# Optimization experiments

Hardware: AMD Instinct MI355X
Metric: run time of the kernel (lower is better)

Reference implementation:

```python
import jax, jax.numpy as jnp
import numpy as np

B, S = 2, 1024
IN, OUT = 1024, 1024
N_IN, N_OUT = 32, 32          # isqrt(IN), isqrt(OUT)
CD = 64                       # compressed_feature_dim
K = 2                         # num_monarchs
D1 = N_IN * N_IN * N_OUT      # 32768, flat M1 size per token
D2 = N_OUT * N_IN * N_OUT     # 32768, flat M2 size per token


def setup_inputs() -> dict:
    key = jax.random.key(0)
    ks = jax.random.split(key, 13)
    g = lambda k, shape, s=0.02: jax.random.normal(k, shape, dtype=jnp.float32) * s
    return {
        "x":  jax.random.normal(ks[0], (B, S, IN), dtype=jnp.float32),
        "Wc": g(ks[1], (IN, CD)),  "bc": g(ks[2], (CD,)),
        "W1": g(ks[3], (K, CD, D1)), "b1": g(ks[4], (K, D1)),
        "W2": g(ks[5], (K, CD, D2)), "b2": g(ks[6], (K, D2)),
        "Wm": g(ks[7], (CD, K)),   "bm": g(ks[8], (K,)),
        "Wb": g(ks[9], (CD, OUT)), "bb": g(ks[10], (OUT,)),
        "Wr": g(ks[11], (CD, 1)),  "br": g(ks[12], (1,)),
    }


def reference(x, Wc, bc, W1, b1, W2, b2, Wm, bm, Wb, bb, Wr, br):
    b, s, _ = x.shape
    # compressor: Linear + Tanh -> [B,S,CD]
    cf = jnp.tanh(x @ Wc + bc)
    # per-expert generated flat weights: [B,S,K,D]
    gen1 = jnp.einsum('bsc,kcd->bskd', cf, W1) + b1
    gen2 = jnp.einsum('bsc,kcd->bskd', cf, W2) + b2
    # expert mixing coefficients -> softmax over K
    coeffs = jax.nn.softmax(cf @ Wm + bm, axis=-1)  # [B,S,K]
    M1f = jnp.einsum('bskd,bsk->bsd', gen1, coeffs)
    M2f = jnp.einsum('bskd,bsk->bsd', gen2, coeffs)
    # Monarch block matmul with per-token weights
    M1 = M1f.reshape(b, s, N_IN, N_IN, N_OUT)   # g=N_IN blocks of [N_IN,N_OUT]
    M2 = M2f.reshape(b, s, N_OUT, N_IN, N_OUT)  # g=N_OUT blocks of [N_IN,N_OUT]
    x1 = x.reshape(b, s, N_IN, N_IN)
    h1 = jnp.einsum('bsgi,bsgio->bsgo', x1, M1)      # [B,S,N_IN,N_OUT]
    h1t = jnp.swapaxes(h1, -1, -2)                   # [B,S,N_OUT,N_IN]
    h2 = jnp.einsum('bsgi,bsgio->bsgo', h1t, M2)     # [B,S,N_OUT,N_OUT]
    y = h2.reshape(b, s, OUT)
    # per-token scale and bias
    ratio = cf @ Wr + br                             # [B,S,1]
    bias = cf @ Wb + bb                              # [B,S,OUT]
    return y * ratio + bias
```

## Files before the change

### kernel.cpp

```cpp
#include <hip/hip_runtime.h>
#include <cstddef>

typedef unsigned short ushortT;
typedef short s8v __attribute__((ext_vector_type(8)));
typedef float f32x4 __attribute__((ext_vector_type(4)));

constexpr int NTOK = 2048;

__device__ inline ushortT f2bf(float f) {
  unsigned u = __float_as_uint(f);
  u += 0x7fffu + ((u >> 16) & 1u);
  return (ushortT)(u >> 16);
}

__device__ inline void gl_lds16(const s8v* g, s8v* l) {
  __builtin_amdgcn_global_load_lds(
      (const __attribute__((address_space(1))) unsigned int*)g,
      (__attribute__((address_space(3))) unsigned int*)l, 16, 0, 0);
}

__global__ __launch_bounds__(256) void setup_kernel(
    const float* __restrict__ x, const float* __restrict__ Wc, const float* __restrict__ bc,
    const float* __restrict__ Wm, const float* __restrict__ bm,
    const float* __restrict__ Wr, const float* __restrict__ br,
    const float* __restrict__ W1, const float* __restrict__ b1,
    const float* __restrict__ W2, const float* __restrict__ b2,
    const float* __restrict__ Wb, const float* __restrict__ bb,
    ushortT* __restrict__ FP, float* __restrict__ ratio,
    ushortT* __restrict__ P1, ushortT* __restrict__ P2, ushortT* __restrict__ WbP)
{
  __shared__ __align__(16) char smem[16384];
  const int tid = threadIdx.x;
  const int bid = blockIdx.x;

  if (bid < 512) {
    float* part = (float*)smem;
    float* cf_s = part + 1024;
    float* a0s  = cf_s + 256;
    float* a1s  = a0s + 4;
    const int c = tid & 63;
    const int q = tid >> 6;
    const int t0 = bid * 4;

    float acc[4];
#pragma unroll
    for (int p = 0; p < 4; ++p) acc[p] = 0.f;
    const float* xq = x + (size_t)t0 * 1024 + q * 256;
    const float* wq = Wc + (size_t)(q * 256) * 64 + c;
#pragma unroll 4
    for (int jj = 0; jj < 64; ++jj) {
      float w0 = wq[(jj * 4 + 0) * 64];
      float w1 = wq[(jj * 4 + 1) * 64];
      float w2 = wq[(jj * 4 + 2) * 64];
      float w3 = wq[(jj * 4 + 3) * 64];
#pragma unroll
      for (int p = 0; p < 4; ++p) {
        float4 xv = *(const float4*)(xq + (size_t)p * 1024 + jj * 4);
        acc[p] = fmaf(xv.x, w0, acc[p]);
        acc[p] = fmaf(xv.y, w1, acc[p]);
        acc[p] = fmaf(xv.z, w2, acc[p]);
        acc[p] = fmaf(xv.w, w3, acc[p]);
      }
    }
#pragma unroll
    for (int p = 0; p < 4; ++p) part[(q * 4 + p) * 64 + c] = acc[p];
    __syncthreads();

    {
      int p = tid >> 6, cc = tid & 63;
      float s = part[(0 + p) * 64 + cc] + part[(4 + p) * 64 + cc] +
                part[(8 + p) * 64 + cc] + part[(12 + p) * 64 + cc] + bc[cc];
      cf_s[p * 64 + cc] = tanhf(s);
    }
    __syncthreads();

    {
      float cf = cf_s[q * 64 + c];
      float z0 = cf * Wm[2 * c], z1 = cf * Wm[2 * c + 1], rr = cf * Wr[c];
      for (int off = 32; off; off >>= 1) {
        z0 += __shfl_down(z0, off);
        z1 += __shfl_down(z1, off);
        rr += __shfl_down(rr, off);
      }
      if (c == 0) {
        z0 += bm[0]; z1 += bm[1];
        float mx = fmaxf(z0, z1);
        float e0 = expf(z0 - mx), e1 = expf(z1 - mx);
        float a0 = e0 / (e0 + e1);
        a0s[q] = a0;
        a1s[q] = 1.0f - a0;
        ratio[t0 + q] = rr + br[0];
      }
    }
    __syncthreads();

    const int ks0 = c >> 5, kk = c & 31;
    const int slot = (kk >> 3) * 16, e = kk & 7;
    {
      int t = t0 + q, tt = t >> 4, tok = t & 15;
      size_t base = (size_t)tt * 2560;
      float cf = cf_s[q * 64 + c];
      float a0 = a0s[q], a1 = a1s[q];
      FP[base + (size_t)ks0 * 512 + (slot + tok) * 8 + e]       = f2bf(a0 * cf);
      FP[base + (size_t)(2 + ks0) * 512 + (slot + tok) * 8 + e] = f2bf(a1 * cf);
      if (c < 32) {
        float v = (c == 0) ? a0 : (c == 1) ? a1 : 0.0f;
        FP[base + 4 * 512 + ((c >> 3) * 16 + tok) * 8 + (c & 7)] = f2bf(v);
      }
    }
  } else {
    ushortT (*lds)[1024] = (ushortT (*)[1024])smem;
    int pb = bid - 512;
    int fac, g, jc8;
    if (pb < 1280) { fac = pb / 640; int rem = pb % 640; g = rem / 20; jc8 = rem % 20; }
    else           { fac = 2; g = 0; jc8 = pb - 1280; }
    const float* W  = (fac == 0) ? W1 : W2;
    const float* bv = (fac == 0) ? b1 : b2;
    ushortT* P = (fac == 0) ? P1 : (fac == 1) ? P2 : WbP;
    const int c4 = tid;

#pragma unroll
    for (int rl = 0; rl < 8; ++rl) {
      int jj = jc8 * 8 + rl;
      float4 v = make_float4(0.f, 0.f, 0.f, 0.f);
      if (fac < 2) {
        if (jj < 128)       v = *(const float4*)(W  + (size_t)jj * 32768 + g * 1024 + c4 * 4);
        else if (jj < 130)  v = *(const float4*)(bv + (size_t)(jj - 128) * 32768 + g * 1024 + c4 * 4);
      } else {
        if (jj < 128)       v = *(const float4*)(Wb + (size_t)(jj & 63) * 1024 + c4 * 4);
        else if (jj < 130)  v = *(const float4*)(bb + c4 * 4);
      }
      int col0 = c4 * 4;
      int sw = col0 ^ ((col0 >> 4) & 0x1C);
      ushortT* d = &lds[rl][sw];
      d[0] = f2bf(v.x); d[1] = f2bf(v.y); d[2] = f2bf(v.z); d[3] = f2bf(v.w);
    }
    __syncthreads();
    const int ks = jc8 >> 2, kkg = jc8 & 3;
#pragma unroll
    for (int it = 0; it < 4; ++it) {
      int idx = tid + it * 256;
      int ct_l = idx >> 4, cl = idx & 15;
      int scol;
      if (fac < 2) {
        int o = ct_l >> 1, ib = (ct_l & 1) * 16;
        scol = (ib + cl) * 32 + o;
      } else {
        scol = ct_l * 16 + cl;
      }
      scol ^= ((scol >> 4) & 0x1C);
      ushortT v[8];
#pragma unroll
      for (int e = 0; e < 8; ++e) v[e] = lds[e][scol];
      size_t ctile = (fac < 2) ? (size_t)(g * 64 + ct_l) : (size_t)ct_l;
      size_t off = ctile * 2560 + (size_t)ks * 512 + (kkg * 16 + cl) * 8;
      uint4 qv;
      qv.x = v[0] | ((unsigned)v[1] << 16);
      qv.y = v[2] | ((unsigned)v[3] << 16);
      qv.z = v[4] | ((unsigned)v[5] << 16);
      qv.w = v[6] | ((unsigned)v[7] << 16);
      *(uint4*)(P + off) = qv;
    }
  }
}

template <int PASS>
__global__ __launch_bounds__(256, 2) void mm_kernel(
    const s8v* __restrict__ fP, const s8v* __restrict__ wP,
    const s8v* __restrict__ wbP,
    const float* __restrict__ xg,
    const float* __restrict__ rat,
    float* __restrict__ outp)
{
  __shared__ s8v bsh[2][1280];
  __shared__ float xsf[(PASS == 1 ? 2 : 1) * 2112];
  __shared__ float hs[PASS == 2 ? 64 : 1][9];
  __shared__ float bls[PASS == 2 ? 64 : 1][9];
  const int tid = threadIdx.x;
  const int lane = tid & 63;
  const int w = tid >> 6;
  const int bid = blockIdx.x;
  const int cb  = (bid & 7) * 16 + (bid >> 5);
  const int tbgh = (bid >> 3) & 3;
  const int g = cb >> 2;

  const s8v* ap = wP + (size_t)(cb * 16 + w * 4) * 320 + lane;
  s8v a[4][5];
#pragma unroll
  for (int i = 0; i < 4; ++i)
#pragma unroll
    for (int ks = 0; ks < 5; ++ks) a[i][ks] = ap[i * 320 + ks * 64];

  s8v ab[5];
  if constexpr (PASS == 2) {
    const s8v* abp = wbP + (size_t)(cb >> 1) * 320 + lane;
#pragma unroll
    for (int ks = 0; ks < 5; ++ks) ab[ks] = abp[ks * 64];
  }

  const s8v* fbase = fP + (size_t)(tbgh * 8) * 1280;

#pragma unroll
  for (int c2 = 0; c2 < 5; ++c2)
    gl_lds16(fbase + w * 320 + c2 * 64 + lane, &bsh[0][w * 320 + c2 * 64]);
  __syncthreads();

#pragma unroll 1
  for (int tt2 = 0; tt2 < 8; ++tt2) {
    const int buf = tt2 & 1;
    const int t0 = (tbgh * 8 + tt2) * 64;

    float4 xv[2];
#pragma unroll
    for (int it = 0; it < 2; ++it) {
      int idx = tid + it * 256;
      if (PASS == 1) {
        int t = idx >> 3, i4 = idx & 7;
        xv[it] = *(const float4*)(xg + (size_t)(t0 + t) * 1024 + g * 32 + i4 * 4);
      } else {
        int i = idx >> 4, tq = idx & 15;
        xv[it] = *(const float4*)(xg + (size_t)(i * 32 + g) * 2048 + t0 + tq * 4);
      }
    }
    if (tt2 < 7) {
      const s8v* fn = fbase + (size_t)(tt2 + 1) * 1280;
#pragma unroll
      for (int c2 = 0; c2 < 5; ++c2)
        gl_lds16(fn + w * 320 + c2 * 64 + lane, &bsh[buf ^ 1][w * 320 + c2 * 64]);
    }

    f32x4 acc[4][4];
#pragma unroll
    for (int i = 0; i < 4; ++i)
#pragma unroll
      for (int j = 0; j < 4; ++j) acc[i][j] = {0.f, 0.f, 0.f, 0.f};
    f32x4 accb = {0.f, 0.f, 0.f, 0.f};

    __builtin_amdgcn_s_setprio(1);
#pragma unroll
    for (int ks = 0; ks < 5; ++ks) {
      s8v b0 = bsh[buf][0 * 320 + ks * 64 + lane];
      s8v b1 = bsh[buf][1 * 320 + ks * 64 + lane];
      s8v b2 = bsh[buf][2 * 320 + ks * 64 + lane];
      s8v b3 = bsh[buf][3 * 320 + ks * 64 + lane];
      if constexpr (PASS == 2) {
        s8v bw = bsh[buf][w * 320 + ks * 64 + lane];
        accb = __builtin_amdgcn_mfma_f32_16x16x32_bf16(ab[ks], bw, accb, 0, 0, 0);
      }
#pragma unroll
      for (int i = 0; i < 4; ++i) {
        acc[i][0] = __builtin_amdgcn_mfma_f32_16x16x32_bf16(a[i][ks], b0, acc[i][0], 0, 0, 0);
        acc[i][1] = __builtin_amdgcn_mfma_f32_16x16x32_bf16(a[i][ks], b1, acc[i][1], 0, 0, 0);
        acc[i][2] = __builtin_amdgcn_mfma_f32_16x16x32_bf16(a[i][ks], b2, acc[i][2], 0, 0, 0);
        acc[i][3] = __builtin_amdgcn_mfma_f32_16x16x32_bf16(a[i][ks], b3, acc[i][3], 0, 0, 0);
      }
    }
    __builtin_amdgcn_s_setprio(0);

#pragma unroll
    for (int it = 0; it < 2; ++it) {
      int idx = tid + it * 256;
      float* d;
      if (PASS == 1) { int t = idx >> 3, i4 = idx & 7; d = &xsf[buf * 2112 + t * 33 + i4 * 4]; }
      else           { int i = idx >> 4, tq = idx & 15; d = &xsf[i * 66 + tq * 4]; }
      d[0] = xv[it].x; d[1] = xv[it].y; d[2] = xv[it].z; d[3] = xv[it].w;
    }
    __syncthreads();

    const int tau = lane & 15, q = lane >> 4;
#pragma unroll
    for (int tt = 0; tt < 4; ++tt) {
      int tl = tt * 16 + tau;
#pragma unroll
      for (int run = 0; run < 2; ++run) {
        float sacc = 0.f;
#pragma unroll
        for (int ch = 0; ch < 2; ++ch) {
          int ct = run * 2 + ch;
          f32x4 av = acc[ct][tt];
#pragma unroll
          for (int r = 0; r < 4; ++r) {
            int i = ch * 16 + q * 4 + r;
            float xvv = (PASS == 1) ? xsf[buf * 2112 + tl * 33 + i] : xsf[i * 66 + tl];
            sacc = fmaf(av[r], xvv, sacc);
          }
        }
        sacc += __shfl_xor(sacc, 16);
        sacc += __shfl_xor(sacc, 32);
        if constexpr (PASS == 1) {
          if (lane < 16) {
            int colg = g * 32 + (cb & 3) * 8 + w * 2 + run;
            outp[(size_t)colg * 2048 + t0 + tt * 16 + tau] = sacc;
          }
        } else {
          if (lane < 16) hs[tl][w * 2 + run] = sacc;
        }
      }
    }
    if constexpr (PASS == 2) {
      if ((lane >> 5) == (cb & 1)) {
        int ol = ((lane >> 4) & 1) * 4;
#pragma unroll
        for (int r = 0; r < 4; ++r) bls[w * 16 + tau][ol + r] = accb[r];
      }
      __syncthreads();
      if (tid < 128) {
        int row = tid >> 1, half = tid & 1;
        int t = t0 + row;
        int col = g * 32 + (cb & 3) * 8 + half * 4;
        float r = rat[t];
        float4 o;
        o.x = fmaf(hs[row][half * 4 + 0], r, bls[row][half * 4 + 0]);
        o.y = fmaf(hs[row][half * 4 + 1], r, bls[row][half * 4 + 1]);
        o.z = fmaf(hs[row][half * 4 + 2], r, bls[row][half * 4 + 2]);
        o.w = fmaf(hs[row][half * 4 + 3], r, bls[row][half * 4 + 3]);
        *(float4*)(outp + (size_t)t * 1024 + col) = o;
      }
    }
  }
}

extern "C" void kernel_launch(void* const* d_in, const int* in_sizes, int n_in,
                              void* d_out, int out_size, void* d_ws, size_t ws_size,
                              hipStream_t stream) {
  const float* x  = (const float*)d_in[0];
  const float* Wc = (const float*)d_in[1];
  const float* bc = (const float*)d_in[2];
  const float* W1 = (const float*)d_in[3];
  const float* b1 = (const float*)d_in[4];
  const float* W2 = (const float*)d_in[5];
  const float* b2 = (const float*)d_in[6];
  const float* Wm = (const float*)d_in[7];
  const float* bm = (const float*)d_in[8];
  const float* Wb = (const float*)d_in[9];
  const float* bb = (const float*)d_in[10];
  const float* Wr = (const float*)d_in[11];
  const float* br = (const float*)d_in[12];
  float* out = (float*)d_out;

  ushortT* P1  = (ushortT*)d_ws;
  ushortT* P2  = P1 + (size_t)2048 * 2560;
  ushortT* WbP = P2 + (size_t)2048 * 2560;
  ushortT* FP  = WbP + (size_t)64 * 2560;
  float* ratio = (float*)(FP + (size_t)128 * 2560);
  float* h1T   = ratio + NTOK;

  setup_kernel<<<dim3(1812), dim3(256), 0, stream>>>(
      x, Wc, bc, Wm, bm, Wr, br, W1, b1, W2, b2, Wb, bb, FP, ratio, P1, P2, WbP);
  mm_kernel<1><<<dim3(512), dim3(256), 0, stream>>>(
      (const s8v*)FP, (const s8v*)P1, (const s8v*)WbP, x, nullptr, h1T);
  mm_kernel<2><<<dim3(512), dim3(256), 0, stream>>>(
      (const s8v*)FP, (const s8v*)P2, (const s8v*)WbP, h1T, ratio, out);
}
```

Before: 77.13 us.

## Move W2 and Wb packing from setup kernel into pass-1 matmul launch

Packing of the W2/b2 and Wb/bb weights into bf16 MFMA tile layout moves out of the setup kernel and into extra blocks appended to the pass-1 matmul grid. The setup grid shrinks, and the W2/Wb packing can run alongside the pass-1 MFMA work, shortening the serial critical path. The pack blocks reuse the matmul's LDS buffer and return early. They compete with matmul blocks for CUs and bandwidth, and the pass-1 grid now contains two kinds of block with very different costs.

```diff
diff --git a/kernel.cpp b/kernel.cpp
--- a/kernel.cpp
+++ b/kernel.cpp
@@ -17,6 +17,57 @@
   __builtin_amdgcn_global_load_lds(
       (const __attribute__((address_space(1))) unsigned int*)g,
       (__attribute__((address_space(3))) unsigned int*)l, 16, 0, 0);
+}
+
+__device__ inline void pack_slab(
+    ushortT (*lds)[1024], int tid, int fac, int g, int jc8,
+    const float* __restrict__ W, const float* __restrict__ bv,
+    const float* __restrict__ Wb, const float* __restrict__ bb,
+    ushortT* __restrict__ P)
+{
+  const int c4 = tid;
+#pragma unroll
+  for (int rl = 0; rl < 8; ++rl) {
+    int jj = jc8 * 8 + rl;
+    float4 v = make_float4(0.f, 0.f, 0.f, 0.f);
+    if (fac < 2) {
+      if (jj < 128)       v = *(const float4*)(W  + (size_t)jj * 32768 + g * 1024 + c4 * 4);
+      else if (jj < 130)  v = *(const float4*)(bv + (size_t)(jj - 128) * 32768 + g * 1024 + c4 * 4);
+    } else {
+      if (jj < 128)       v = *(const float4*)(Wb + (size_t)(jj & 63) * 1024 + c4 * 4);
+      else if (jj < 130)  v = *(const float4*)(bb + c4 * 4);
+    }
+    int col0 = c4 * 4;
+    int sw = col0 ^ ((col0 >> 4) & 0x1C);
+    ushortT* d = &lds[rl][sw];
+    d[0] = f2bf(v.x); d[1] = f2bf(v.y); d[2] = f2bf(v.z); d[3] = f2bf(v.w);
+  }
+  __syncthreads();
+  const int ks = jc8 >> 2, kkg = jc8 & 3;
+#pragma unroll
+  for (int it = 0; it < 4; ++it) {
+    int idx = tid + it * 256;
+    int ct_l = idx >> 4, cl = idx & 15;
+    int scol;
+    if (fac < 2) {
+      int o = ct_l >> 1, ib = (ct_l & 1) * 16;
+      scol = (ib + cl) * 32 + o;
+    } else {
+      scol = ct_l * 16 + cl;
+    }
+    scol ^= ((scol >> 4) & 0x1C);
+    ushortT v[8];
+#pragma unroll
+    for (int e = 0; e < 8; ++e) v[e] = lds[e][scol];
+    size_t ctile = (fac < 2) ? (size_t)(g * 64 + ct_l) : (size_t)ct_l;
+    size_t off = ctile * 2560 + (size_t)ks * 512 + (kkg * 16 + cl) * 8;
+    uint4 qv;
+    qv.x = v[0] | ((unsigned)v[1] << 16);
+    qv.y = v[2] | ((unsigned)v[3] << 16);
+    qv.z = v[4] | ((unsigned)v[5] << 16);
+    qv.w = v[6] | ((unsigned)v[7] << 16);
+    *(uint4*)(P + off) = qv;
+  }
 }
 
 __global__ __launch_bounds__(256) void setup_kernel(
@@ -24,10 +75,7 @@
     const float* __restrict__ Wm, const float* __restrict__ bm,
     const float* __restrict__ Wr, const float* __restrict__ br,
     const float* __restrict__ W1, const float* __restrict__ b1,
-    const float* __restrict__ W2, const float* __restrict__ b2,
-    const float* __restrict__ Wb, const float* __restrict__ bb,
-    ushortT* __restrict__ FP, float* __restrict__ ratio,
-    ushortT* __restrict__ P1, ushortT* __restrict__ P2, ushortT* __restrict__ WbP)
+    ushortT* __restrict__ FP, float* __restrict__ ratio, ushortT* __restrict__ P1)
 {
   __shared__ __align__(16) char smem[16384];
   const int tid = threadIdx.x;
@@ -111,56 +159,7 @@
   } else {
     ushortT (*lds)[1024] = (ushortT (*)[1024])smem;
     int pb = bid - 512;
-    int fac, g, jc8;
-    if (pb < 1280) { fac = pb / 640; int rem = pb % 640; g = rem / 20; jc8 = rem % 20; }
-    else           { fac = 2; g = 0; jc8 = pb - 1280; }
-    const float* W  = (fac == 0) ? W1 : W2;
-    const float* bv = (fac == 0) ? b1 : b2;
-    ushortT* P = (fac == 0) ? P1 : (fac == 1) ? P2 : WbP;
-    const int c4 = tid;
-
-#pragma unroll
-    for (int rl = 0; rl < 8; ++rl) {
-      int jj = jc8 * 8 + rl;
-      float4 v = make_float4(0.f, 0.f, 0.f, 0.f);
-      if (fac < 2) {
-        if (jj < 128)       v = *(const float4*)(W  + (size_t)jj * 32768 + g * 1024 + c4 * 4);
-        else if (jj < 130)  v = *(const float4*)(bv + (size_t)(jj - 128) * 32768 + g * 1024 + c4 * 4);
-      } else {
-        if (jj < 128)       v = *(const float4*)(Wb + (size_t)(jj & 63) * 1024 + c4 * 4);
-        else if (jj < 130)  v = *(const float4*)(bb + c4 * 4);
-      }
-      int col0 = c4 * 4;
-      int sw = col0 ^ ((col0 >> 4) & 0x1C);
-      ushortT* d = &lds[rl][sw];
-      d[0] = f2bf(v.x); d[1] = f2bf(v.y); d[2] = f2bf(v.z); d[3] = f2bf(v.w);
-    }
-    __syncthreads();
-    const int ks = jc8 >> 2, kkg = jc8 & 3;
-#pragma unroll
-    for (int it = 0; it < 4; ++it) {
-      int idx = tid + it * 256;
-      int ct_l = idx >> 4, cl = idx & 15;
-      int scol;
-      if (fac < 2) {
-        int o = ct_l >> 1, ib = (ct_l & 1) * 16;
-        scol = (ib + cl) * 32 + o;
-      } else {
-        scol = ct_l * 16 + cl;
-      }
-      scol ^= ((scol >> 4) & 0x1C);
-      ushortT v[8];
-#pragma unroll
-      for (int e = 0; e < 8; ++e) v[e] = lds[e][scol];
-      size_t ctile = (fac < 2) ? (size_t)(g * 64 + ct_l) : (size_t)ct_l;
-      size_t off = ctile * 2560 + (size_t)ks * 512 + (kkg * 16 + cl) * 8;
-      uint4 qv;
-      qv.x = v[0] | ((unsigned)v[1] << 16);
-      qv.y = v[2] | ((unsigned)v[3] << 16);
-      qv.z = v[4] | ((unsigned)v[5] << 16);
-      qv.w = v[6] | ((unsigned)v[7] << 16);
-      *(uint4*)(P + off) = qv;
-    }
+    pack_slab(lds, tid, 0, pb / 20, pb % 20, W1, b1, nullptr, nullptr, P1);
   }
 }
 
@@ -170,16 +169,30 @@
     const s8v* __restrict__ wbP,
     const float* __restrict__ xg,
     const float* __restrict__ rat,
-    float* __restrict__ outp)
+    float* __restrict__ outp,
+    const float* __restrict__ W2, const float* __restrict__ b2,
+    const float* __restrict__ Wb, const float* __restrict__ bb,
+    ushortT* __restrict__ P2, ushortT* __restrict__ WbPo)
 {
   __shared__ s8v bsh[2][1280];
   __shared__ float xsf[(PASS == 1 ? 2 : 1) * 2112];
   __shared__ float hs[PASS == 2 ? 64 : 1][9];
   __shared__ float bls[PASS == 2 ? 64 : 1][9];
   const int tid = threadIdx.x;
+  const int bid = blockIdx.x;
+
+  if constexpr (PASS == 1) {
+    if (bid >= 512) {
+      ushortT (*lds)[1024] = (ushortT (*)[1024])&bsh[0][0];
+      int pb = bid - 512;
+      if (pb < 640) pack_slab(lds, tid, 1, pb / 20, pb % 20, W2, b2, nullptr, nullptr, P2);
+      else          pack_slab(lds, tid, 2, 0, pb - 640, nullptr, nullptr, Wb, bb, WbPo);
+      return;
+    }
+  }
+
   const int lane = tid & 63;
   const int w = tid >> 6;
-  const int bid = blockIdx.x;
   const int cb  = (bid & 7) * 16 + (bid >> 5);
   const int tbgh = (bid >> 3) & 3;
   const int g = cb >> 2;
@@ -241,7 +254,7 @@
     for (int ks = 0; ks < 5; ++ks) {
       s8v b0 = bsh[buf][0 * 320 + ks * 64 + lane];
       s8v b1 = bsh[buf][1 * 320 + ks * 64 + lane];
-      s8v b2 = bsh[buf][2 * 320 + ks * 64 + lane];
+      s8v b2v = bsh[buf][2 * 320 + ks * 64 + lane];
       s8v b3 = bsh[buf][3 * 320 + ks * 64 + lane];
       if constexpr (PASS == 2) {
         s8v bw = bsh[buf][w * 320 + ks * 64 + lane];
@@ -249,10 +262,10 @@
       }
 #pragma unroll
       for (int i = 0; i < 4; ++i) {
-        acc[i][0] = __builtin_amdgcn_mfma_f32_16x16x32_bf16(a[i][ks], b0, acc[i][0], 0, 0, 0);
-        acc[i][1] = __builtin_amdgcn_mfma_f32_16x16x32_bf16(a[i][ks], b1, acc[i][1], 0, 0, 0);
-        acc[i][2] = __builtin_amdgcn_mfma_f32_16x16x32_bf16(a[i][ks], b2, acc[i][2], 0, 0, 0);
-        acc[i][3] = __builtin_amdgcn_mfma_f32_16x16x32_bf16(a[i][ks], b3, acc[i][3], 0, 0, 0);
+        acc[i][0] = __builtin_amdgcn_mfma_f32_16x16x32_bf16(a[i][ks], b0,  acc[i][0], 0, 0, 0);
+        acc[i][1] = __builtin_amdgcn_mfma_f32_16x16x32_bf16(a[i][ks], b1,  acc[i][1], 0, 0, 0);
+        acc[i][2] = __builtin_amdgcn_mfma_f32_16x16x32_bf16(a[i][ks], b2v, acc[i][2], 0, 0, 0);
+        acc[i][3] = __builtin_amdgcn_mfma_f32_16x16x32_bf16(a[i][ks], b3,  acc[i][3], 0, 0, 0);
       }
     }
     __builtin_amdgcn_s_setprio(0);
@@ -345,10 +358,12 @@
   float* ratio = (float*)(FP + (size_t)128 * 2560);
   float* h1T   = ratio + NTOK;
 
-  setup_kernel<<<dim3(1812), dim3(256), 0, stream>>>(
-      x, Wc, bc, Wm, bm, Wr, br, W1, b1, W2, b2, Wb, bb, FP, ratio, P1, P2, WbP);
-  mm_kernel<1><<<dim3(512), dim3(256), 0, stream>>>(
-      (const s8v*)FP, (const s8v*)P1, (const s8v*)WbP, x, nullptr, h1T);
+  setup_kernel<<<dim3(1152), dim3(256), 0, stream>>>(
+      x, Wc, bc, Wm, bm, Wr, br, W1, b1, FP, ratio, P1);
+  mm_kernel<1><<<dim3(1172), dim3(256), 0, stream>>>(
+      (const s8v*)FP, (const s8v*)P1, (const s8v*)WbP, x, nullptr, h1T,
+      W2, b2, Wb, bb, P2, WbP);
   mm_kernel<2><<<dim3(512), dim3(256), 0, stream>>>(
-      (const s8v*)FP, (const s8v*)P2, (const s8v*)WbP, h1T, ratio, out);
-}
+      (const s8v*)FP, (const s8v*)P2, (const s8v*)WbP, h1T, ratio, out,
+      nullptr, nullptr, nullptr, nullptr, nullptr, nullptr);
+}
```

Result: no change. 77.51 us (+0.5%).
